# Kernel tuning notes

Hardware: AMD Instinct MI355X
Metric: run time of the kernel (lower is better)

Reference implementation:

```python
import jax, jax.numpy as jnp
import numpy as np

BATCH, SEQ, N_INPUT, N_HIDDEN, N_OUTPUT = 256, 512, 512, 128, 2


def setup_inputs() -> dict:
    key = jax.random.key(0)
    ks = jax.random.split(key, 6)
    s_i = 1.0 / np.sqrt(N_INPUT)
    s_h = 1.0 / np.sqrt(N_HIDDEN)
    return {
        "x": jax.random.normal(ks[0], (BATCH, SEQ, N_INPUT), dtype=jnp.float32),
        # LSTM gate kernels, gate order (i, f, g, o) concatenated on last axis.
        # flax nn.LSTMCell: dense_i has no bias, dense_h has bias.
        "Wi": jax.random.normal(ks[1], (N_INPUT, 4 * N_HIDDEN), dtype=jnp.float32) * s_i,
        "Wh": jax.random.normal(ks[2], (N_HIDDEN, 4 * N_HIDDEN), dtype=jnp.float32) * s_h,
        "b": jax.random.normal(ks[3], (4 * N_HIDDEN,), dtype=jnp.float32) * 0.01,
        "Wd": jax.random.normal(ks[4], (N_HIDDEN, N_OUTPUT), dtype=jnp.float32) * s_h,
        "bd": jax.random.normal(ks[5], (N_OUTPUT,), dtype=jnp.float32) * 0.01,
    }


def reference(x, Wi, Wh, b, Wd, bd):
    B, S, _ = x.shape
    H = Wh.shape[0]
    # Precompute input projection for all steps in one big GEMM: (S, B, 4H)
    x_gates = jnp.einsum('bsi,ig->sbg', x, Wi)

    def step(carry, xg):
        c, h = carry
        gates = xg + h @ Wh + b  # (B, 4H)
        i, f, g, o = jnp.split(gates, 4, axis=-1)
        c = jax.nn.sigmoid(f) * c + jax.nn.sigmoid(i) * jnp.tanh(g)
        h = jax.nn.sigmoid(o) * jnp.tanh(c)
        return (c, h), h

    c0 = jnp.zeros((B, H), dtype=x.dtype)
    h0 = jnp.zeros((B, H), dtype=x.dtype)
    (_, h_last), _ = jax.lax.scan(step, (c0, h0), x_gates)
    logits = h_last @ Wd + bd  # (B, N_OUTPUT)
    return logits
```

## Files before the change

### kernel.cpp

```cpp
#include <hip/hip_runtime.h>
#include <hip/hip_bf16.h>


typedef __attribute__((ext_vector_type(8))) short short8;
typedef __attribute__((ext_vector_type(4))) float floatx4;
typedef __attribute__((ext_vector_type(4))) unsigned short ushortx4;
typedef __attribute__((ext_vector_type(2))) unsigned int uint2v;

#define LOG2E 1.44269504088896340736f
#define NPROD 192
#define HBS 152
#define HBUF (16 * HBS)

__device__ __forceinline__ unsigned short f2bf(float f) {
  unsigned int u = __builtin_bit_cast(unsigned int, f);
  u = (u + 0x7fffu + ((u >> 16) & 1u)) >> 16;
  return (unsigned short)u;
}
__device__ __forceinline__ float bf2f(unsigned short u) {
  unsigned int v = ((unsigned int)u) << 16;
  return __builtin_bit_cast(float, v);
}
__device__ __forceinline__ float sigf(float x) {
  return __builtin_amdgcn_rcpf(1.0f + __builtin_amdgcn_exp2f(-LOG2E * x));
}
__device__ __forceinline__ float tanhf_(float x) {
  return 1.0f - 2.0f * __builtin_amdgcn_rcpf(1.0f + __builtin_amdgcn_exp2f(2.0f * LOG2E * x));
}
__device__ __forceinline__ void bar_lds() {
  asm volatile("s_waitcnt lgkmcnt(0)" ::: "memory");
  __builtin_amdgcn_s_barrier();
  __builtin_amdgcn_sched_barrier(0);
}
__device__ __forceinline__ void gl_lds16(const void* g, void* l) {
  __builtin_amdgcn_global_load_lds(
      (const __attribute__((address_space(1))) unsigned int*)g,
      (__attribute__((address_space(3))) unsigned int*)l, 16, 0, 0);
}

__global__ void pack_kernel(const float* __restrict__ Wi, const float* __restrict__ Wh,
                            unsigned short* __restrict__ Wi_p, unsigned short* __restrict__ Wh_p,
                            unsigned int* __restrict__ flags) {
  if (blockIdx.x == 0 && threadIdx.x < 8) flags[threadIdx.x] = 0u;
  int idx = blockIdx.x * 256 + threadIdx.x;
  if (idx < 262144) {
    int j = idx & 7, lane = (idx >> 3) & 63, nt = (idx >> 9) & 31, kk = idx >> 14;
    int k = kk * 32 + ((lane >> 4) * 8) + j;
    int n = nt * 16 + (lane & 15);
    Wi_p[idx] = f2bf(Wi[k * 512 + n]);
  } else {
    int i2 = idx - 262144;
    int j = i2 & 7, lane = (i2 >> 3) & 63, nt = (i2 >> 9) & 31, kk = i2 >> 14;
    int k = kk * 32 + ((lane >> 4) * 8) + j;
    int n = nt * 16 + (lane & 15);
    Wh_p[i2] = f2bf(Wh[k * 512 + n]);
  }
}

__global__ __launch_bounds__(512, 2) void fused_kernel(
    const float* __restrict__ x, const unsigned short* __restrict__ Wi_p,
    const float* __restrict__ bias, unsigned int* __restrict__ xg5,
    const unsigned short* __restrict__ Wh_p, const float* __restrict__ Wd,
    const float* __restrict__ bd, float* __restrict__ out,
    unsigned int* __restrict__ flags) {
  __shared__ __align__(16) unsigned short As[128 * 72];
  __shared__ __align__(16) unsigned short Bs[2 * 32 * 64 * 8];
  __shared__ __align__(16) unsigned short hb[2 * HBUF];

  const int tid = threadIdx.x;
  const int lane = tid & 63;
  const int w = tid >> 6;
  const int quad = lane >> 4;
  const int lm = lane & 15;

  if (blockIdx.x < NPROD) {
    const int wm = w >> 2, wn = w & 3;

    float bs_[4][2];
    #pragma unroll
    for (int g = 0; g < 4; ++g)
      #pragma unroll
      for (int jc = 0; jc < 2; ++jc)
        bs_[g][jc] = bias[g * 128 + wn * 32 + jc * 16 + lm];

    for (int t = blockIdx.x; t < 1024; t += NPROD) {
      const int s = t >> 1;
      const int b0 = (t & 1) * 128;

      floatx4 acc[4][8];
      #pragma unroll
      for (int a = 0; a < 4; ++a)
        #pragma unroll
        for (int b2 = 0; b2 < 8; ++b2) { acc[a][b2].x = 0.f; acc[a][b2].y = 0.f; acc[a][b2].z = 0.f; acc[a][b2].w = 0.f; }

      const float* xbase = x + ((size_t)(b0 + w * 16 + quad) * 512 + s) * 512 + lm * 4;

      floatx4 cur[4], nxt[4];
      #pragma unroll
      for (int i = 0; i < 4; ++i)
        cur[i] = *(const floatx4*)(xbase + (size_t)i * 1048576);

      for (int kt = 0; kt < 8; ++kt) {
        bar_lds();
        #pragma unroll
        for (int i = 0; i < 4; ++i) {
          int r = w * 16 + i * 4 + quad;
          ushortx4 u;
          u.x = f2bf(cur[i].x); u.y = f2bf(cur[i].y); u.z = f2bf(cur[i].z); u.w = f2bf(cur[i].w);
          *(ushortx4*)(&As[r * 72 + lm * 4]) = u;
        }
        #pragma unroll
        for (int c = 0; c < 8; ++c) {
          int kg = c & 1, ntl = (c >> 1) * 8 + w;
          const unsigned short* src = Wi_p + ((size_t)((kt * 2 + kg) * 32 + ntl) * 64 + lane) * 8;
          unsigned short* dst = &Bs[(size_t)((kg * 32 + ntl) * 64) * 8];
          gl_lds16(src, dst);
        }
        __builtin_amdgcn_sched_barrier(0);
        if (kt < 7) {
          #pragma unroll
          for (int i = 0; i < 4; ++i)
            nxt[i] = *(const floatx4*)(xbase + (size_t)i * 1048576 + (kt + 1) * 64);
          asm volatile("s_waitcnt vmcnt(4) lgkmcnt(0)" ::: "memory");
        } else {
          asm volatile("s_waitcnt vmcnt(0) lgkmcnt(0)" ::: "memory");
        }
        __builtin_amdgcn_s_barrier();
        __builtin_amdgcn_sched_barrier(0);
        #pragma unroll
        for (int ks = 0; ks < 2; ++ks) {
          short8 af[4];
          #pragma unroll
          for (int mt = 0; mt < 4; ++mt) {
            int m = wm * 64 + mt * 16 + lm;
            af[mt] = *(const short8*)(&As[m * 72 + ks * 32 + quad * 8]);
          }
          #pragma unroll
          for (int nt = 0; nt < 8; ++nt) {
            int g = nt >> 1, jc = nt & 1;
            int ntl = g * 8 + wn * 2 + jc;
            short8 bfv = *(const short8*)(&Bs[(size_t)((ks * 32 + ntl) * 64 + lane) * 8]);
            #pragma unroll
            for (int mt = 0; mt < 4; ++mt)
              acc[mt][nt] = __builtin_amdgcn_mfma_f32_16x16x32_bf16(af[mt], bfv, acc[mt][nt], 0, 0, 0);
          }
        }
        #pragma unroll
        for (int i = 0; i < 4; ++i) cur[i] = nxt[i];
      }
      #pragma unroll
      for (int mt = 0; mt < 4; ++mt) {
        int bbase = b0 + wm * 64 + mt * 16 + quad * 4;
        #pragma unroll
        for (int jc = 0; jc < 2; ++jc) {
          int wv = wn * 2 + jc;
          #pragma unroll
          for (int rr = 0; rr < 4; ++rr) {
            size_t cell = ((size_t)s * 64 + ((bbase + rr) >> 2)) * 512 + wv * 64 + rr * 16 + lm;
            float g0 = acc[mt][0 + jc][rr] + bs_[0][jc];
            float g1 = acc[mt][2 + jc][rr] + bs_[1][jc];
            float g2 = acc[mt][4 + jc][rr] + bs_[2][jc];
            float g3 = acc[mt][6 + jc][rr] + bs_[3][jc];
            unsigned long long v64 =
                (unsigned long long)((unsigned int)f2bf(g0) | ((unsigned int)f2bf(g1) << 16)) |
                ((unsigned long long)((unsigned int)f2bf(g2) | ((unsigned int)f2bf(g3) << 16)) << 32);
            __hip_atomic_store((unsigned long long*)xg5 + cell, v64,
                               __ATOMIC_RELAXED, __HIP_MEMORY_SCOPE_AGENT);
          }
        }
      }
      __syncthreads();
      __builtin_amdgcn_sched_barrier(0);
      if (tid == 0)
        __hip_atomic_fetch_add(&flags[t >> 7], 1u, __ATOMIC_RELEASE, __HIP_MEMORY_SCOPE_AGENT);
    }
  } else {
    const int bb = blockIdx.x - NPROD;

    for (int i = tid; i < 2 * HBUF; i += 512) hb[i] = 0;

    short8 bfr[4][4];
    #pragma unroll
    for (int kk = 0; kk < 4; ++kk)
      #pragma unroll
      for (int g = 0; g < 4; ++g)
        bfr[kk][g] = *(const short8*)(Wh_p + ((size_t)(kk * 32 + g * 8 + w) * 64 + lane) * 8);

    float cst[4] = {0.f, 0.f, 0.f, 0.f};
    const bool act = (lm < 4);

    const unsigned long long* xp =
        (const unsigned long long*)xg5 + ((size_t)bb * 512 + w * 64 + lm * 16 + quad * 4);

    auto at_load8 = [](const unsigned long long* p) -> unsigned long long {
      return __hip_atomic_load(p, __ATOMIC_RELAXED, __HIP_MEMORY_SCOPE_AGENT);
    };

    __syncthreads();

    unsigned long long xga[4], xgb[4];

    auto substep = [&](const int rp, unsigned long long (&xc)[4], int spre) {
      unsigned long long xv[4];
      #pragma unroll
      for (int r = 0; r < 4; ++r) xv[r] = xc[r];

      short8 af[4];
      #pragma unroll
      for (int kk = 0; kk < 4; ++kk)
        af[kk] = *(const short8*)(&hb[rp * HBUF + lm * HBS + kk * 32 + quad * 8]);

      if (spre < 512 && act) {
        #pragma unroll
        for (int r = 0; r < 4; ++r)
          xc[r] = at_load8(xp + (size_t)spre * 32768 + r);
      }

      floatx4 acc[4];
      #pragma unroll
      for (int g = 0; g < 4; ++g) { acc[g].x = 0.f; acc[g].y = 0.f; acc[g].z = 0.f; acc[g].w = 0.f; }
      #pragma unroll
      for (int kk = 0; kk < 4; ++kk)
        #pragma unroll
        for (int g = 0; g < 4; ++g)
          acc[g] = __builtin_amdgcn_mfma_f32_16x16x32_bf16(bfr[kk][g], af[kk], acc[g], 0, 0, 0);

      unsigned short hv[4];
      #pragma unroll
      for (int r = 0; r < 4; ++r) {
        float pre0 = acc[0][r] + bf2f((unsigned short)(xv[r] & 0xffffu));
        float pre1 = acc[1][r] + bf2f((unsigned short)((xv[r] >> 16) & 0xffffu));
        float pre2 = acc[2][r] + bf2f((unsigned short)((xv[r] >> 32) & 0xffffu));
        float pre3 = acc[3][r] + bf2f((unsigned short)(xv[r] >> 48));
        float cc = sigf(pre1) * cst[r] + sigf(pre0) * tanhf_(pre2);
        cst[r] = cc;
        hv[r] = f2bf(sigf(pre3) * tanhf_(cc));
      }
      if (act) {
        ushortx4 hv4;
        hv4.x = hv[0]; hv4.y = hv[1]; hv4.z = hv[2]; hv4.w = hv[3];
        *(ushortx4*)(&hb[(rp ^ 1) * HBUF + lm * HBS + w * 16 + quad * 4]) = hv4;
      }
      bar_lds();
    };

    for (int c = 0; c < 8; ++c) {
      if (w == 0) {
        while (__hip_atomic_load(&flags[c], __ATOMIC_RELAXED, __HIP_MEMORY_SCOPE_AGENT) < 128u)
          __builtin_amdgcn_s_sleep(2);
      }
      bar_lds();
      if (act) {
        #pragma unroll
        for (int r = 0; r < 4; ++r) {
          xga[r] = at_load8(xp + (size_t)(c * 64) * 32768 + r);
          xgb[r] = at_load8(xp + (size_t)(c * 64 + 1) * 32768 + r);
        }
      }
      #pragma unroll 1
      for (int s2 = 0; s2 < 64; s2 += 2) {
        int s = c * 64 + s2;
        substep(0, xga, s + 2);
        substep(1, xgb, s + 3);
      }
    }

    if (tid < 8) {
      int rw = tid >> 1, co = tid & 1;
      float a = bd[co];
      for (int j2 = 0; j2 < 128; ++j2)
        a += bf2f(hb[rw * HBS + j2]) * Wd[j2 * 2 + co];
      out[(bb * 4 + rw) * 2 + co] = a;
    }
  }
}

extern "C" void kernel_launch(void* const* d_in, const int* in_sizes, int n_in,
                              void* d_out, int out_size, void* d_ws, size_t ws_size,
                              hipStream_t stream) {
  const float* x  = (const float*)d_in[0];
  const float* Wi = (const float*)d_in[1];
  const float* Wh = (const float*)d_in[2];
  const float* b  = (const float*)d_in[3];
  const float* Wd = (const float*)d_in[4];
  const float* bd = (const float*)d_in[5];
  float* out = (float*)d_out;

  unsigned short* Wi_p = (unsigned short*)d_ws;
  unsigned short* Wh_p = Wi_p + 262144;
  unsigned int*   flags = (unsigned int*)(Wh_p + 65536);
  unsigned int*   xg5  = flags + 128;

  pack_kernel<<<1280, 256, 0, stream>>>(Wi, Wh, Wi_p, Wh_p, flags);
  fused_kernel<<<256, 512, 0, stream>>>(x, Wi_p, b, xg5, Wh_p, Wd, bd, out, flags);
}
```

Baseline: 823.1 us.

## Pack 16 batch rows per recurrent block and use more producer blocks

The recurrent consumer blocks now swap the MFMA operand roles so each 16-row tile carries 16 batch rows instead of 4. That removes the idle lanes masked off by `act` and cuts the number of recurrent blocks. The freed CUs go to more producer blocks for the input-projection GEMM (NPROD 240). The K reduction is also split into two independent accumulator chains to shorten the dependent MFMA chain per step. The price is a new xgates and hidden-state indexing layout, scalar LDS stores, and heavier per-block recurrent work, all relying on the grid launch matching the new batch mapping.

```diff
diff --git a/kernel.cpp b/kernel.cpp
--- a/kernel.cpp
+++ b/kernel.cpp
@@ -8,7 +8,7 @@
 typedef __attribute__((ext_vector_type(2))) unsigned int uint2v;
 
 #define LOG2E 1.44269504088896340736f
-#define NPROD 192
+#define NPROD 240
 #define HBS 152
 #define HBUF (16 * HBS)
 
@@ -187,10 +187,9 @@
         bfr[kk][g] = *(const short8*)(Wh_p + ((size_t)(kk * 32 + g * 8 + w) * 64 + lane) * 8);
 
     float cst[4] = {0.f, 0.f, 0.f, 0.f};
-    const bool act = (lm < 4);
 
     const unsigned long long* xp =
-        (const unsigned long long*)xg5 + ((size_t)bb * 512 + w * 64 + lm * 16 + quad * 4);
+        (const unsigned long long*)xg5 + ((size_t)(bb * 4 + quad) * 512 + w * 64 + lm);
 
     auto at_load8 = [](const unsigned long long* p) -> unsigned long long {
       return __hip_atomic_load(p, __ATOMIC_RELAXED, __HIP_MEMORY_SCOPE_AGENT);
@@ -210,37 +209,44 @@
       for (int kk = 0; kk < 4; ++kk)
         af[kk] = *(const short8*)(&hb[rp * HBUF + lm * HBS + kk * 32 + quad * 8]);
 
-      if (spre < 512 && act) {
+      if (spre < 512) {
         #pragma unroll
         for (int r = 0; r < 4; ++r)
-          xc[r] = at_load8(xp + (size_t)spre * 32768 + r);
-      }
-
-      floatx4 acc[4];
-      #pragma unroll
-      for (int g = 0; g < 4; ++g) { acc[g].x = 0.f; acc[g].y = 0.f; acc[g].z = 0.f; acc[g].w = 0.f; }
-      #pragma unroll
-      for (int kk = 0; kk < 4; ++kk)
-        #pragma unroll
-        for (int g = 0; g < 4; ++g)
-          acc[g] = __builtin_amdgcn_mfma_f32_16x16x32_bf16(bfr[kk][g], af[kk], acc[g], 0, 0, 0);
+          xc[r] = at_load8(xp + (size_t)spre * 32768 + r * 16);
+      }
+
+      floatx4 accA[4], accB[4];
+      #pragma unroll
+      for (int g = 0; g < 4; ++g) {
+        accA[g].x = 0.f; accA[g].y = 0.f; accA[g].z = 0.f; accA[g].w = 0.f;
+        accB[g].x = 0.f; accB[g].y = 0.f; accB[g].z = 0.f; accB[g].w = 0.f;
+      }
+      #pragma unroll
+      for (int g = 0; g < 4; ++g) {
+        accA[g] = __builtin_amdgcn_mfma_f32_16x16x32_bf16(af[0], bfr[0][g], accA[g], 0, 0, 0);
+        accB[g] = __builtin_amdgcn_mfma_f32_16x16x32_bf16(af[2], bfr[2][g], accB[g], 0, 0, 0);
+        accA[g] = __builtin_amdgcn_mfma_f32_16x16x32_bf16(af[1], bfr[1][g], accA[g], 0, 0, 0);
+        accB[g] = __builtin_amdgcn_mfma_f32_16x16x32_bf16(af[3], bfr[3][g], accB[g], 0, 0, 0);
+      }
 
       unsigned short hv[4];
       #pragma unroll
       for (int r = 0; r < 4; ++r) {
-        float pre0 = acc[0][r] + bf2f((unsigned short)(xv[r] & 0xffffu));
-        float pre1 = acc[1][r] + bf2f((unsigned short)((xv[r] >> 16) & 0xffffu));
-        float pre2 = acc[2][r] + bf2f((unsigned short)((xv[r] >> 32) & 0xffffu));
-        float pre3 = acc[3][r] + bf2f((unsigned short)(xv[r] >> 48));
+        float g0 = accA[0][r] + accB[0][r];
+        float g1 = accA[1][r] + accB[1][r];
+        float g2 = accA[2][r] + accB[2][r];
+        float g3 = accA[3][r] + accB[3][r];
+        float pre0 = g0 + bf2f((unsigned short)(xv[r] & 0xffffu));
+        float pre1 = g1 + bf2f((unsigned short)((xv[r] >> 16) & 0xffffu));
+        float pre2 = g2 + bf2f((unsigned short)((xv[r] >> 32) & 0xffffu));
+        float pre3 = g3 + bf2f((unsigned short)(xv[r] >> 48));
         float cc = sigf(pre1) * cst[r] + sigf(pre0) * tanhf_(pre2);
         cst[r] = cc;
         hv[r] = f2bf(sigf(pre3) * tanhf_(cc));
       }
-      if (act) {
-        ushortx4 hv4;
-        hv4.x = hv[0]; hv4.y = hv[1]; hv4.z = hv[2]; hv4.w = hv[3];
-        *(ushortx4*)(&hb[(rp ^ 1) * HBUF + lm * HBS + w * 16 + quad * 4]) = hv4;
-      }
+      #pragma unroll
+      for (int r = 0; r < 4; ++r)
+        hb[(rp ^ 1) * HBUF + (quad * 4 + r) * HBS + w * 16 + lm] = hv[r];
       bar_lds();
     };
 
@@ -250,12 +256,10 @@
           __builtin_amdgcn_s_sleep(2);
       }
       bar_lds();
-      if (act) {
-        #pragma unroll
-        for (int r = 0; r < 4; ++r) {
-          xga[r] = at_load8(xp + (size_t)(c * 64) * 32768 + r);
-          xgb[r] = at_load8(xp + (size_t)(c * 64 + 1) * 32768 + r);
-        }
+      #pragma unroll
+      for (int r = 0; r < 4; ++r) {
+        xga[r] = at_load8(xp + (size_t)(c * 64) * 32768 + r * 16);
+        xgb[r] = at_load8(xp + (size_t)(c * 64 + 1) * 32768 + r * 16);
       }
       #pragma unroll 1
       for (int s2 = 0; s2 < 64; s2 += 2) {
@@ -265,12 +269,12 @@
       }
     }
 
-    if (tid < 8) {
+    if (tid < 32) {
       int rw = tid >> 1, co = tid & 1;
       float a = bd[co];
       for (int j2 = 0; j2 < 128; ++j2)
         a += bf2f(hb[rw * HBS + j2]) * Wd[j2 * 2 + co];
-      out[(bb * 4 + rw) * 2 + co] = a;
+      out[(bb * 16 + rw) * 2 + co] = a;
     }
   }
 }
```

Measured after the change: 855.0 us. +3.9%, slower.
